# Kernel tuning notes

Measured on AMD Instinct MI355X. Metric: run time of the kernel, lower is better.

## Reference

```python
import jax, jax.numpy as jnp
import numpy as np

V = 512          # num vertices
F = 64           # pair-feature dim (gpnn_channels in)
C = 64           # gpnn_channels out
E = 8192         # num edges (avg degree 16)


def setup_inputs() -> dict:
    key = jax.random.key(0)
    k1, k2, k3, k4 = jax.random.split(key, 4)
    alpha = jax.random.normal(k1, (V * V, F), dtype=jnp.float32)          # pair features, row v*V+w
    edge_index = jax.random.randint(k2, (2, E), 0, V)                      # COO [src; dst]
    # GPNNEdgeConv.nn = MLP([F, C, C], act='relu')  (norm treated as identity / eval stats)
    w1 = jax.random.normal(k3, (F, C), dtype=jnp.float32) * (1.0 / np.sqrt(F))
    b1 = jnp.zeros((C,), dtype=jnp.float32)
    w2 = jax.random.normal(k4, (C, C), dtype=jnp.float32) * (1.0 / np.sqrt(C))
    b2 = jnp.zeros((C,), dtype=jnp.float32)
    eps = jnp.asarray(0.0, dtype=jnp.float32)                              # train_eps parameter
    return {"alpha": alpha, "edge_index": edge_index,
            "w1": w1, "b1": b1, "w2": w2, "b2": b2, "eps": eps}


def reference(alpha, edge_index, w1, b1, w2, b2, eps):
    # Dense 0/1 adjacency adj_t: adj[v, j] = 1 iff edge j -> v (dst-indexed, as spmm(adj_t, .)).
    adj = jnp.zeros((V, V), dtype=alpha.dtype).at[edge_index[1], edge_index[0]].set(1.0)
    a3 = alpha.reshape(V, V, F)  # a3[v, j] = alpha[v*V + j]
    # message_and_aggregate: out[v*V+w] = row v of spmm(adj_t, A_{v,w}),
    # where A_{v,w}[j] = alpha[v*V+j] + alpha[w*V+j]  (sum aggregation)
    #   = sum_j adj[v,j] * (a3[v,j] + a3[w,j]) = S[v] + T[v,w]
    S = jnp.einsum('vj,vjf->vf', adj, a3)    # [V, F]
    T = jnp.einsum('vj,wjf->vwf', adj, a3)   # [V, V, F]
    out = (S[:, None, :] + T).reshape(V * V, F)
    # GINConv residual: out + (1 + eps) * x_r, then MLP (Linear-ReLU-Linear)
    out = out + (1.0 + eps) * alpha
    h = jax.nn.relu(out @ w1 + b1)
    return h @ w2 + b2
```

## Files before the change

### kernel.cpp

```cpp
#include <hip/hip_runtime.h>
#include <hip/hip_bf16.h>

#define NV 512
#define NF 64

typedef __attribute__((ext_vector_type(8))) short bf16x8;
typedef __attribute__((ext_vector_type(4))) float f32x4;

union BF8 { bf16x8 v; unsigned u[4]; };

__device__ __forceinline__ unsigned cvt2(float lo, float hi) {
    __hip_bfloat162 p = __float22bfloat162_rn(float2{lo, hi});
    return *reinterpret_cast<unsigned*>(&p);
}
__device__ __forceinline__ unsigned short cvt1(float x) {
    __hip_bfloat16 b = __float2bfloat16(x);
    return *reinterpret_cast<unsigned short*>(&b);
}

__device__ __forceinline__ unsigned awt_addr(int f, int jbyte) {
    return (unsigned)((f * 1024 + jbyte) ^ (((f ^ (f >> 3)) & 7) << 4));
}
__device__ __forceinline__ int slot2(int row) {
    return 2 * (((row >> 2) ^ row) & 3) + (row & 1);
}

__global__ void k_edges(const int* __restrict__ ei, int E, unsigned int* __restrict__ mask) {
    int e = blockIdx.x * 256 + threadIdx.x;
    if (e < E) {
        int s = ei[e];
        int d = ei[E + e];
        atomicOr(&mask[d * 16 + (s >> 5)], 1u << (s & 31));
    }
}

__global__ void k_wprep(const float* __restrict__ w1, const float* __restrict__ w2,
                        unsigned short* __restrict__ wfrag) {
    int t = threadIdx.x;
#pragma unroll
    for (int it = 0; it < 4; ++it) {
        int item = it * 256 + t;
        int lanei = item & 63;
        int nt = (item >> 6) & 3;
        int ks = (item >> 8) & 1;
        int m  = item >> 9;
        const float* wsrc = m ? w2 : w1;
        int n = nt * 16 + (lanei & 15);
        int k0 = ks * 32 + (lanei >> 4) * 8;
        BF8 p;
#pragma unroll
        for (int h = 0; h < 4; ++h)
            p.u[h] = cvt2(wsrc[(k0 + 2 * h) * NF + n], wsrc[(k0 + 2 * h + 1) * NF + n]);
        *(bf16x8*)(wfrag + (size_t)item * 8) = p.v;
    }
}

__global__ void k_S(const unsigned int* __restrict__ mask, const float* __restrict__ alpha,
                    float* __restrict__ S) {
    __shared__ float red[4][64];
    int v = blockIdx.x;
    int lane = threadIdx.x & 63;
    int g = threadIdx.x >> 6;
    float a0 = 0.f, a1 = 0.f;
    for (int wd = g * 4; wd < g * 4 + 4; ++wd) {
        unsigned bits = mask[v * 16 + wd];
        while (bits) {
            int b0 = __ffs(bits) - 1; bits &= bits - 1;
            float x0 = alpha[((size_t)v * NV + wd * 32 + b0) * NF + lane];
            if (bits) {
                int b1 = __ffs(bits) - 1; bits &= bits - 1;
                a1 += alpha[((size_t)v * NV + wd * 32 + b1) * NF + lane];
            }
            a0 += x0;
        }
    }
    red[g][lane] = a0 + a1;
    __syncthreads();
    if (g == 0)
        S[v * NF + lane] = red[0][lane] + red[1][lane] + red[2][lane] + red[3][lane];
}

__global__ __launch_bounds__(512, 2) void k_main(
    const float* __restrict__ alpha, const unsigned short* __restrict__ wfrag,
    const float* __restrict__ b1, const float* __restrict__ b2,
    const float* __restrict__ eps_p,
    const unsigned int* __restrict__ mask, const float* __restrict__ S,
    float* __restrict__ out)
{
    extern __shared__ char smem[];
    const int w    = blockIdx.x;
    const int t    = threadIdx.x;
    const int lane = t & 63;
    const int wid  = t >> 6;
    const int nlo  = lane & 15;
    const int g    = lane >> 4;
    const int mbase = wid * 64;
    const float* src = alpha + (size_t)w * (NV * NF);

    auto stage_half = [&](int i) {
        int task = i * 512 + t;
        int jb = task >> 4;
        int fq = task & 15;
        unsigned ua[4][4];
#pragma unroll
        for (int h = 0; h < 4; ++h) {
            f32x4 r0 = *(const f32x4*)(src + (size_t)(jb * 8 + 2 * h) * NF + fq * 4);
            f32x4 r1 = *(const f32x4*)(src + (size_t)(jb * 8 + 2 * h + 1) * NF + fq * 4);
#pragma unroll
            for (int c = 0; c < 4; ++c)
                ua[c][h] = cvt2(r0[c], r1[c]);
        }
#pragma unroll
        for (int c = 0; c < 4; ++c) {
            BF8 p;
            p.u[0] = ua[c][0]; p.u[1] = ua[c][1]; p.u[2] = ua[c][2]; p.u[3] = ua[c][3];
            *(bf16x8*)(smem + awt_addr(fq * 4 + c, jb * 16)) = p.v;
        }
    };

    f32x4 acc[4][4];

    stage_half(0);

    uint4 qm[4][4];
#pragma unroll
    for (int mi = 0; mi < 4; ++mi)
#pragma unroll
        for (int kq = 0; kq < 4; ++kq)
            qm[mi][kq] = *(const uint4*)(mask + (size_t)(mbase + mi * 16 + nlo) * 16 + kq * 4);

#pragma unroll
    for (int mi = 0; mi < 4; ++mi)
#pragma unroll
        for (int nt = 0; nt < 4; ++nt)
#pragma unroll
            for (int r = 0; r < 4; ++r)
                acc[mi][nt][r] = S[(size_t)(mbase + mi * 16 + g * 4 + r) * NF + nt * 16 + nlo];

    __syncthreads();

    auto gemm_q = [&](int kq) {
#pragma unroll
        for (int kr = 0; kr < 4; ++kr) {
            const int kk = kq * 4 + kr;
            const unsigned wv[4] = {
                (&qm[0][kq].x)[kr], (&qm[1][kq].x)[kr],
                (&qm[2][kq].x)[kr], (&qm[3][kq].x)[kr] };
            BF8 afr[4];
#pragma unroll
            for (int mi = 0; mi < 4; ++mi) {
                unsigned byteb = (wv[mi] >> (g * 8)) & 0xFFu;
#pragma unroll
                for (int h = 0; h < 4; ++h) {
                    unsigned b0 = (byteb >> (2 * h)) & 1u;
                    unsigned b1 = (byteb >> (2 * h + 1)) & 1u;
                    afr[mi].u[h] = (b0 ? 0x3F80u : 0u) | (b1 ? 0x3F800000u : 0u);
                }
            }
#pragma unroll
            for (int nt = 0; nt < 4; ++nt) {
                bf16x8 bfr = *(const bf16x8*)(smem + awt_addr(nt * 16 + nlo, kk * 64 + g * 16));
#pragma unroll
                for (int mi = 0; mi < 4; ++mi)
                    acc[mi][nt] = __builtin_amdgcn_mfma_f32_16x16x32_bf16(afr[mi].v, bfr, acc[mi][nt], 0, 0, 0);
            }
        }
    };

    stage_half(1);
    gemm_q(0); gemm_q(1);
    __syncthreads();
    gemm_q(2); gemm_q(3);

    bf16x8 w1f[2][4], w2f[2][4];
#pragma unroll
    for (int ks = 0; ks < 2; ++ks)
#pragma unroll
        for (int nt = 0; nt < 4; ++nt) {
            w1f[ks][nt] = *(const bf16x8*)(wfrag + (size_t)(((0 * 2 + ks) * 4 + nt) * 64 + lane) * 8);
            w2f[ks][nt] = *(const bf16x8*)(wfrag + (size_t)(((1 * 2 + ks) * 4 + nt) * 64 + lane) * 8);
        }
    float b1v[4], b2v[4];
#pragma unroll
    for (int nt = 0; nt < 4; ++nt) {
        b1v[nt] = b1[nt * 16 + nlo];
        b2v[nt] = b2[nt * 16 + nlo];
    }
    const float ceps = 1.0f + eps_p[0];

    __syncthreads();

    char* myscr = smem + wid * 2048;
#pragma unroll
    for (int mi = 0; mi < 4; ++mi) {
        int v0 = mbase + mi * 16;
        float rvv[4][4];
#pragma unroll
        for (int nt = 0; nt < 4; ++nt)
#pragma unroll
            for (int r = 0; r < 4; ++r)
                rvv[nt][r] = alpha[((size_t)(v0 + g * 4 + r) * NV + w) * NF + nt * 16 + nlo];
#pragma unroll
        for (int nt = 0; nt < 4; ++nt)
#pragma unroll
            for (int r = 0; r < 4; ++r) {
                float pre = acc[mi][nt][r] + ceps * rvv[nt][r];
                int row = g * 4 + r;
                *(unsigned short*)(myscr + row * 128 + ((2 * (nt * 16 + nlo)) ^ (slot2(row) << 4))) = cvt1(pre);
            }

        bf16x8 a0 = *(const bf16x8*)(myscr + nlo * 128 + ((g * 16) ^ (slot2(nlo) << 4)));
        bf16x8 a1 = *(const bf16x8*)(myscr + nlo * 128 + ((g * 16 + 64) ^ (slot2(nlo) << 4)));
        f32x4 accm[4];
#pragma unroll
        for (int nt = 0; nt < 4; ++nt) {
            f32x4 z = {0.f, 0.f, 0.f, 0.f};
            z = __builtin_amdgcn_mfma_f32_16x16x32_bf16(a0, w1f[0][nt], z, 0, 0, 0);
            z = __builtin_amdgcn_mfma_f32_16x16x32_bf16(a1, w1f[1][nt], z, 0, 0, 0);
            accm[nt] = z;
        }

#pragma unroll
        for (int nt = 0; nt < 4; ++nt)
#pragma unroll
            for (int r = 0; r < 4; ++r) {
                float hv = accm[nt][r] + b1v[nt];
                hv = hv > 0.f ? hv : 0.f;
                int row = g * 4 + r;
                *(unsigned short*)(myscr + row * 128 + ((2 * (nt * 16 + nlo)) ^ (slot2(row) << 4))) = cvt1(hv);
            }

        bf16x8 h0 = *(const bf16x8*)(myscr + nlo * 128 + ((g * 16) ^ (slot2(nlo) << 4)));
        bf16x8 h1 = *(const bf16x8*)(myscr + nlo * 128 + ((g * 16 + 64) ^ (slot2(nlo) << 4)));
#pragma unroll
        for (int nt = 0; nt < 4; ++nt) {
            f32x4 z = {0.f, 0.f, 0.f, 0.f};
            z = __builtin_amdgcn_mfma_f32_16x16x32_bf16(h0, w2f[0][nt], z, 0, 0, 0);
            z = __builtin_amdgcn_mfma_f32_16x16x32_bf16(h1, w2f[1][nt], z, 0, 0, 0);
#pragma unroll
            for (int r = 0; r < 4; ++r) {
                int vv = v0 + g * 4 + r;
                out[((size_t)vv * NV + w) * NF + nt * 16 + nlo] = z[r] + b2v[nt];
            }
        }
    }
}

extern "C" void kernel_launch(void* const* d_in, const int* in_sizes, int n_in,
                              void* d_out, int out_size, void* d_ws, size_t ws_size,
                              hipStream_t stream) {
    const float* alpha = (const float*)d_in[0];
    const int*   ei    = (const int*)d_in[1];
    const float* w1    = (const float*)d_in[2];
    const float* b1    = (const float*)d_in[3];
    const float* w2    = (const float*)d_in[4];
    const float* b2    = (const float*)d_in[5];
    const float* eps   = (const float*)d_in[6];
    float* out = (float*)d_out;
    int E = in_sizes[1] / 2;

    unsigned int*   mask  = (unsigned int*)d_ws;
    float*          S     = (float*)((char*)d_ws + 32768);
    unsigned short* wfrag = (unsigned short*)((char*)d_ws + 32768 + 131072);

    hipMemsetAsync(mask, 0, 32768, stream);
    k_edges<<<(E + 255) / 256, 256, 0, stream>>>(ei, E, mask);
    k_wprep<<<1, 256, 0, stream>>>(w1, w2, wfrag);
    k_S    <<<NV, 256, 0, stream>>>(mask, alpha, S);

    hipFuncSetAttribute(reinterpret_cast<const void*>(k_main),
                        hipFuncAttributeMaxDynamicSharedMemorySize, 65536);
    k_main<<<NV, 512, 65536, stream>>>(alpha, wfrag, b1, b2, eps, mask, S, out);
}
```

Measured before the change: 65.49 us.

## Process two w columns per block with double-buffered LDS staging

Each block now handles two consecutive w indices, with a 128 KB LDS allocation split into two staging regions. The second column's alpha slice is converted and staged while the first column's adjacency GEMM runs, and the grid is halved to match. Mask fragments are now reloaded per k-quarter instead of held in registers for the whole GEMM, which lowers register pressure. The cost is that only one block fits per CU because of the larger LDS footprint, so latency hiding drops, and the second column's work runs serially after the first.

Result: slower. 100.2 us (+53.0%).

```diff
diff --git a/kernel.cpp b/kernel.cpp
--- a/kernel.cpp
+++ b/kernel.cpp
@@ -88,162 +88,169 @@
     float* __restrict__ out)
 {
     extern __shared__ char smem[];
-    const int w    = blockIdx.x;
+    const int bid  = blockIdx.x;
     const int t    = threadIdx.x;
     const int lane = t & 63;
     const int wid  = t >> 6;
     const int nlo  = lane & 15;
     const int g    = lane >> 4;
     const int mbase = wid * 64;
-    const float* src = alpha + (size_t)w * (NV * NF);
-
-    auto stage_half = [&](int i) {
-        int task = i * 512 + t;
-        int jb = task >> 4;
-        int fq = task & 15;
-        unsigned ua[4][4];
-#pragma unroll
-        for (int h = 0; h < 4; ++h) {
-            f32x4 r0 = *(const f32x4*)(src + (size_t)(jb * 8 + 2 * h) * NF + fq * 4);
-            f32x4 r1 = *(const f32x4*)(src + (size_t)(jb * 8 + 2 * h + 1) * NF + fq * 4);
-#pragma unroll
-            for (int c = 0; c < 4; ++c)
-                ua[c][h] = cvt2(r0[c], r1[c]);
-        }
-#pragma unroll
-        for (int c = 0; c < 4; ++c) {
-            BF8 p;
-            p.u[0] = ua[c][0]; p.u[1] = ua[c][1]; p.u[2] = ua[c][2]; p.u[3] = ua[c][3];
-            *(bf16x8*)(smem + awt_addr(fq * 4 + c, jb * 16)) = p.v;
+    const int w0 = 2 * bid, w1 = 2 * bid + 1;
+    char* regA = smem;
+    char* regB = smem + 65536;
+    const float ceps = 1.0f + eps_p[0];
+
+    auto stage = [&](char* region, int w) {
+        const float* src = alpha + (size_t)w * (NV * NF);
+#pragma unroll
+        for (int i = 0; i < 2; ++i) {
+            int task = i * 512 + t;
+            int jb = task >> 4;
+            int fq = task & 15;
+            unsigned ua[4][4];
+#pragma unroll
+            for (int h = 0; h < 4; ++h) {
+                f32x4 r0 = *(const f32x4*)(src + (size_t)(jb * 8 + 2 * h) * NF + fq * 4);
+                f32x4 r1 = *(const f32x4*)(src + (size_t)(jb * 8 + 2 * h + 1) * NF + fq * 4);
+#pragma unroll
+                for (int c = 0; c < 4; ++c)
+                    ua[c][h] = cvt2(r0[c], r1[c]);
+            }
+#pragma unroll
+            for (int c = 0; c < 4; ++c) {
+                BF8 p;
+                p.u[0] = ua[c][0]; p.u[1] = ua[c][1]; p.u[2] = ua[c][2]; p.u[3] = ua[c][3];
+                *(bf16x8*)(region + awt_addr(fq * 4 + c, jb * 16)) = p.v;
+            }
         }
     };
 
     f32x4 acc[4][4];
 
-    stage_half(0);
-
-    uint4 qm[4][4];
-#pragma unroll
-    for (int mi = 0; mi < 4; ++mi)
-#pragma unroll
-        for (int kq = 0; kq < 4; ++kq)
-            qm[mi][kq] = *(const uint4*)(mask + (size_t)(mbase + mi * 16 + nlo) * 16 + kq * 4);
-
-#pragma unroll
-    for (int mi = 0; mi < 4; ++mi)
-#pragma unroll
-        for (int nt = 0; nt < 4; ++nt)
-#pragma unroll
-            for (int r = 0; r < 4; ++r)
-                acc[mi][nt][r] = S[(size_t)(mbase + mi * 16 + g * 4 + r) * NF + nt * 16 + nlo];
-
+    auto init_acc = [&]() {
+#pragma unroll
+        for (int mi = 0; mi < 4; ++mi)
+#pragma unroll
+            for (int nt = 0; nt < 4; ++nt)
+#pragma unroll
+                for (int r = 0; r < 4; ++r)
+                    acc[mi][nt][r] = S[(size_t)(mbase + mi * 16 + g * 4 + r) * NF + nt * 16 + nlo];
+    };
+
+    auto gemm_all = [&](char* region) {
+#pragma unroll
+        for (int kq = 0; kq < 4; ++kq) {
+            uint4 qm[4];
+#pragma unroll
+            for (int mi = 0; mi < 4; ++mi)
+                qm[mi] = *(const uint4*)(mask + (size_t)(mbase + mi * 16 + nlo) * 16 + kq * 4);
+#pragma unroll
+            for (int kr = 0; kr < 4; ++kr) {
+                const int kk = kq * 4 + kr;
+                BF8 afr[4];
+#pragma unroll
+                for (int mi = 0; mi < 4; ++mi) {
+                    unsigned byteb = ((&qm[mi].x)[kr] >> (g * 8)) & 0xFFu;
+#pragma unroll
+                    for (int h = 0; h < 4; ++h) {
+                        unsigned b0 = (byteb >> (2 * h)) & 1u;
+                        unsigned b1 = (byteb >> (2 * h + 1)) & 1u;
+                        afr[mi].u[h] = (b0 ? 0x3F80u : 0u) | (b1 ? 0x3F800000u : 0u);
+                    }
+                }
+#pragma unroll
+                for (int nt = 0; nt < 4; ++nt) {
+                    bf16x8 bfr = *(const bf16x8*)(region + awt_addr(nt * 16 + nlo, kk * 64 + g * 16));
+#pragma unroll
+                    for (int mi = 0; mi < 4; ++mi)
+                        acc[mi][nt] = __builtin_amdgcn_mfma_f32_16x16x32_bf16(afr[mi].v, bfr, acc[mi][nt], 0, 0, 0);
+                }
+            }
+        }
+    };
+
+    auto epilogue = [&](int w) {
+        bf16x8 w1f[2][4], w2f[2][4];
+#pragma unroll
+        for (int ks = 0; ks < 2; ++ks)
+#pragma unroll
+            for (int nt = 0; nt < 4; ++nt) {
+                w1f[ks][nt] = *(const bf16x8*)(wfrag + (size_t)((ks * 4 + nt) * 64 + lane) * 8);
+                w2f[ks][nt] = *(const bf16x8*)(wfrag + (size_t)(((2 + ks) * 4 + nt) * 64 + lane) * 8);
+            }
+        float b1v[4], b2v[4];
+#pragma unroll
+        for (int nt = 0; nt < 4; ++nt) {
+            b1v[nt] = b1[nt * 16 + nlo];
+            b2v[nt] = b2[nt * 16 + nlo];
+        }
+        char* myscr = regA + wid * 2048;
+#pragma unroll
+        for (int mi = 0; mi < 4; ++mi) {
+            int v0 = mbase + mi * 16;
+            float rvv[4][4];
+#pragma unroll
+            for (int nt = 0; nt < 4; ++nt)
+#pragma unroll
+                for (int r = 0; r < 4; ++r)
+                    rvv[nt][r] = alpha[((size_t)(v0 + g * 4 + r) * NV + w) * NF + nt * 16 + nlo];
+#pragma unroll
+            for (int nt = 0; nt < 4; ++nt)
+#pragma unroll
+                for (int r = 0; r < 4; ++r) {
+                    float pre = acc[mi][nt][r] + ceps * rvv[nt][r];
+                    int row = g * 4 + r;
+                    *(unsigned short*)(myscr + row * 128 + ((2 * (nt * 16 + nlo)) ^ (slot2(row) << 4))) = cvt1(pre);
+                }
+
+            bf16x8 a0 = *(const bf16x8*)(myscr + nlo * 128 + ((g * 16) ^ (slot2(nlo) << 4)));
+            bf16x8 a1 = *(const bf16x8*)(myscr + nlo * 128 + ((g * 16 + 64) ^ (slot2(nlo) << 4)));
+            f32x4 accm[4];
+#pragma unroll
+            for (int nt = 0; nt < 4; ++nt) {
+                f32x4 z = {0.f, 0.f, 0.f, 0.f};
+                z = __builtin_amdgcn_mfma_f32_16x16x32_bf16(a0, w1f[0][nt], z, 0, 0, 0);
+                z = __builtin_amdgcn_mfma_f32_16x16x32_bf16(a1, w1f[1][nt], z, 0, 0, 0);
+                accm[nt] = z;
+            }
+#pragma unroll
+            for (int nt = 0; nt < 4; ++nt)
+#pragma unroll
+                for (int r = 0; r < 4; ++r) {
+                    float hv = accm[nt][r] + b1v[nt];
+                    hv = hv > 0.f ? hv : 0.f;
+                    int row = g * 4 + r;
+                    *(unsigned short*)(myscr + row * 128 + ((2 * (nt * 16 + nlo)) ^ (slot2(row) << 4))) = cvt1(hv);
+                }
+            bf16x8 h0 = *(const bf16x8*)(myscr + nlo * 128 + ((g * 16) ^ (slot2(nlo) << 4)));
+            bf16x8 h1 = *(const bf16x8*)(myscr + nlo * 128 + ((g * 16 + 64) ^ (slot2(nlo) << 4)));
+#pragma unroll
+            for (int nt = 0; nt < 4; ++nt) {
+                f32x4 z = {0.f, 0.f, 0.f, 0.f};
+                z = __builtin_amdgcn_mfma_f32_16x16x32_bf16(h0, w2f[0][nt], z, 0, 0, 0);
+                z = __builtin_amdgcn_mfma_f32_16x16x32_bf16(h1, w2f[1][nt], z, 0, 0, 0);
+#pragma unroll
+                for (int r = 0; r < 4; ++r) {
+                    int vv = v0 + g * 4 + r;
+                    out[((size_t)vv * NV + w) * NF + nt * 16 + nlo] = z[r] + b2v[nt];
+                }
+            }
+        }
+    };
+
+    stage(regA, w0);
+    init_acc();
     __syncthreads();
 
-    auto gemm_q = [&](int kq) {
-#pragma unroll
-        for (int kr = 0; kr < 4; ++kr) {
-            const int kk = kq * 4 + kr;
-            const unsigned wv[4] = {
-                (&qm[0][kq].x)[kr], (&qm[1][kq].x)[kr],
-                (&qm[2][kq].x)[kr], (&qm[3][kq].x)[kr] };
-            BF8 afr[4];
-#pragma unroll
-            for (int mi = 0; mi < 4; ++mi) {
-                unsigned byteb = (wv[mi] >> (g * 8)) & 0xFFu;
-#pragma unroll
-                for (int h = 0; h < 4; ++h) {
-                    unsigned b0 = (byteb >> (2 * h)) & 1u;
-                    unsigned b1 = (byteb >> (2 * h + 1)) & 1u;
-                    afr[mi].u[h] = (b0 ? 0x3F80u : 0u) | (b1 ? 0x3F800000u : 0u);
-                }
-            }
-#pragma unroll
-            for (int nt = 0; nt < 4; ++nt) {
-                bf16x8 bfr = *(const bf16x8*)(smem + awt_addr(nt * 16 + nlo, kk * 64 + g * 16));
-#pragma unroll
-                for (int mi = 0; mi < 4; ++mi)
-                    acc[mi][nt] = __builtin_amdgcn_mfma_f32_16x16x32_bf16(afr[mi].v, bfr, acc[mi][nt], 0, 0, 0);
-            }
-        }
-    };
-
-    stage_half(1);
-    gemm_q(0); gemm_q(1);
+    stage(regB, w1);
+    gemm_all(regA);
     __syncthreads();
-    gemm_q(2); gemm_q(3);
-
-    bf16x8 w1f[2][4], w2f[2][4];
-#pragma unroll
-    for (int ks = 0; ks < 2; ++ks)
-#pragma unroll
-        for (int nt = 0; nt < 4; ++nt) {
-            w1f[ks][nt] = *(const bf16x8*)(wfrag + (size_t)(((0 * 2 + ks) * 4 + nt) * 64 + lane) * 8);
-            w2f[ks][nt] = *(const bf16x8*)(wfrag + (size_t)(((1 * 2 + ks) * 4 + nt) * 64 + lane) * 8);
-        }
-    float b1v[4], b2v[4];
-#pragma unroll
-    for (int nt = 0; nt < 4; ++nt) {
-        b1v[nt] = b1[nt * 16 + nlo];
-        b2v[nt] = b2[nt * 16 + nlo];
-    }
-    const float ceps = 1.0f + eps_p[0];
-
-    __syncthreads();
-
-    char* myscr = smem + wid * 2048;
-#pragma unroll
-    for (int mi = 0; mi < 4; ++mi) {
-        int v0 = mbase + mi * 16;
-        float rvv[4][4];
-#pragma unroll
-        for (int nt = 0; nt < 4; ++nt)
-#pragma unroll
-            for (int r = 0; r < 4; ++r)
-                rvv[nt][r] = alpha[((size_t)(v0 + g * 4 + r) * NV + w) * NF + nt * 16 + nlo];
-#pragma unroll
-        for (int nt = 0; nt < 4; ++nt)
-#pragma unroll
-            for (int r = 0; r < 4; ++r) {
-                float pre = acc[mi][nt][r] + ceps * rvv[nt][r];
-                int row = g * 4 + r;
-                *(unsigned short*)(myscr + row * 128 + ((2 * (nt * 16 + nlo)) ^ (slot2(row) << 4))) = cvt1(pre);
-            }
-
-        bf16x8 a0 = *(const bf16x8*)(myscr + nlo * 128 + ((g * 16) ^ (slot2(nlo) << 4)));
-        bf16x8 a1 = *(const bf16x8*)(myscr + nlo * 128 + ((g * 16 + 64) ^ (slot2(nlo) << 4)));
-        f32x4 accm[4];
-#pragma unroll
-        for (int nt = 0; nt < 4; ++nt) {
-            f32x4 z = {0.f, 0.f, 0.f, 0.f};
-            z = __builtin_amdgcn_mfma_f32_16x16x32_bf16(a0, w1f[0][nt], z, 0, 0, 0);
-            z = __builtin_amdgcn_mfma_f32_16x16x32_bf16(a1, w1f[1][nt], z, 0, 0, 0);
-            accm[nt] = z;
-        }
-
-#pragma unroll
-        for (int nt = 0; nt < 4; ++nt)
-#pragma unroll
-            for (int r = 0; r < 4; ++r) {
-                float hv = accm[nt][r] + b1v[nt];
-                hv = hv > 0.f ? hv : 0.f;
-                int row = g * 4 + r;
-                *(unsigned short*)(myscr + row * 128 + ((2 * (nt * 16 + nlo)) ^ (slot2(row) << 4))) = cvt1(hv);
-            }
-
-        bf16x8 h0 = *(const bf16x8*)(myscr + nlo * 128 + ((g * 16) ^ (slot2(nlo) << 4)));
-        bf16x8 h1 = *(const bf16x8*)(myscr + nlo * 128 + ((g * 16 + 64) ^ (slot2(nlo) << 4)));
-#pragma unroll
-        for (int nt = 0; nt < 4; ++nt) {
-            f32x4 z = {0.f, 0.f, 0.f, 0.f};
-            z = __builtin_amdgcn_mfma_f32_16x16x32_bf16(h0, w2f[0][nt], z, 0, 0, 0);
-            z = __builtin_amdgcn_mfma_f32_16x16x32_bf16(h1, w2f[1][nt], z, 0, 0, 0);
-#pragma unroll
-            for (int r = 0; r < 4; ++r) {
-                int vv = v0 + g * 4 + r;
-                out[((size_t)vv * NV + w) * NF + nt * 16 + nlo] = z[r] + b2v[nt];
-            }
-        }
-    }
+
+    epilogue(w0);
+
+    init_acc();
+    gemm_all(regB);
+    epilogue(w1);
 }
 
 extern "C" void kernel_launch(void* const* d_in, const int* in_sizes, int n_in,
@@ -269,6 +276,6 @@
     k_S    <<<NV, 256, 0, stream>>>(mask, alpha, S);
 
     hipFuncSetAttribute(reinterpret_cast<const void*>(k_main),
-                        hipFuncAttributeMaxDynamicSharedMemorySize, 65536);
-    k_main<<<NV, 512, 65536, stream>>>(alpha, wfrag, b1, b2, eps, mask, S, out);
-}
+                        hipFuncAttributeMaxDynamicSharedMemorySize, 131072);
+    k_main<<<NV / 2, 512, 131072, stream>>>(alpha, wfrag, b1, b2, eps, mask, S, out);
+}
```
